# Kernel optimization log

Hardware: AMD Instinct MI355X
Metric: run time of the kernel (lower is better)

The kernel has to match this reference:

```python
import jax, jax.numpy as jnp
import numpy as np

N = 100000
E = 1600000
F_IN = 128
HID = 64
HID2 = 32
NCLS = 2
EPS = 1e-5  # BatchNorm eps


def setup_inputs() -> dict:
    key = jax.random.key(0)
    ks = jax.random.split(key, 12)
    inp = {
        'x': jax.random.normal(ks[0], (N, F_IN), dtype=jnp.float32),
        'edge_index': jax.random.randint(ks[1], (2, E), 0, N, dtype=jnp.int64),
        # GCNConv layer 1: weight [F_IN, HID], bias [HID]
        'W1': jax.random.normal(ks[2], (F_IN, HID), dtype=jnp.float32) / np.sqrt(F_IN),
        'b1': jnp.zeros((HID,), dtype=jnp.float32),
        # GCNConv layer 2
        'W2': jax.random.normal(ks[3], (HID, HID2), dtype=jnp.float32) / np.sqrt(HID),
        'b2': jnp.zeros((HID2,), dtype=jnp.float32),
        # BatchNorm1d params (eval mode: running stats)
        'g1': jax.random.uniform(ks[4], (HID,), dtype=jnp.float32, minval=0.5, maxval=1.5),
        'be1': jax.random.normal(ks[5], (HID,), dtype=jnp.float32) * 0.1,
        'rm1': jax.random.normal(ks[6], (HID,), dtype=jnp.float32) * 0.1,
        'rv1': jax.random.uniform(ks[7], (HID,), dtype=jnp.float32, minval=0.5, maxval=1.5),
        'g2': jax.random.uniform(ks[8], (HID2,), dtype=jnp.float32, minval=0.5, maxval=1.5),
        'be2': jax.random.normal(ks[9], (HID2,), dtype=jnp.float32) * 0.1,
        'rm2': jax.random.normal(ks[10], (HID2,), dtype=jnp.float32) * 0.1,
        'rv2': jax.random.uniform(ks[11], (HID2,), dtype=jnp.float32, minval=0.5, maxval=1.5),
        # classifier
        'Wc': jax.random.normal(jax.random.fold_in(key, 99), (HID2, NCLS), dtype=jnp.float32) / np.sqrt(HID2),
        'bc': jnp.zeros((NCLS,), dtype=jnp.float32),
    }
    return inp


def _gcn_conv(x, src, dst, norm, W, b, n_nodes):
    # PyG GCNConv: transform -> gather source -> norm-weight -> scatter-add -> +bias
    h = x @ W                                  # [N, out]
    msg = h[src] * norm[:, None]               # [E+N, out] gathered messages
    out = jax.ops.segment_sum(msg, dst, num_segments=n_nodes)
    return out + b


def _bn_eval(x, gamma, beta, rmean, rvar):
    return (x - rmean) * (gamma * jax.lax.rsqrt(rvar + EPS)) + beta


def reference(x, edge_index, W1, b1, W2, b2, g1, be1, rm1, rv1, g2, be2, rm2, rv2, Wc, bc):
    n = x.shape[0]
    loop = jnp.arange(n, dtype=edge_index.dtype)
    src = jnp.concatenate([edge_index[0], loop])   # add self-loops
    dst = jnp.concatenate([edge_index[1], loop])
    # symmetric degree normalization on A + I (degree counted at target)
    deg = jax.ops.segment_sum(jnp.ones_like(dst, dtype=x.dtype), dst, num_segments=n)
    dinv = jnp.where(deg > 0, jax.lax.rsqrt(deg), 0.0)
    norm = dinv[src] * dinv[dst]                   # [E+N]

    h = _gcn_conv(x, src, dst, norm, W1, b1, n)
    h = jax.nn.relu(_bn_eval(h, g1, be1, rm1, rv1))
    # dropout: identity in eval mode
    h = _gcn_conv(h, src, dst, norm, W2, b2, n)
    h = jax.nn.relu(_bn_eval(h, g2, be2, rm2, rv2))
    logits = h @ Wc + bc
    return jax.nn.log_softmax(logits, axis=1)
```

## Files before the change

kernel.cpp:

```cpp
#include <hip/hip_runtime.h>
#include <hip/hip_fp16.h>
#include <math.h>

#define F_IN 128
#define HID 64
#define HID2 32
#define EPS_BN 1e-5f
#define BW 128
#define NBMAX 1024
#define CAP 2560
#define CH 8192

__global__ __launch_bounds__(1024) void partition_kernel(const int* __restrict__ src, const int* __restrict__ dst,
                                                         int E, int* __restrict__ gcursor,
                                                         unsigned* __restrict__ ebuf) {
    __shared__ int hist[NBMAX];
    __shared__ int start[NBMAX];
    __shared__ int cur[NBMAX];
    __shared__ int gb[NBMAX];
    __shared__ int sc[1024];
    __shared__ unsigned buf[CH];
    int tid = threadIdx.x;
    int e0 = blockIdx.x * CH;
    hist[tid] = 0;
    __syncthreads();
#pragma unroll
    for (int it = 0; it < CH / 1024; it++) {
        int e = e0 + tid + it * 1024;
        if (e < E) atomicAdd(&hist[dst[e] >> 7], 1);
    }
    __syncthreads();
    int v = hist[tid];
    sc[tid] = v;
    __syncthreads();
    for (int off = 1; off < 1024; off <<= 1) {
        int t = (tid >= off) ? sc[tid - off] : 0;
        __syncthreads();
        sc[tid] += t;
        __syncthreads();
    }
    int ex = sc[tid] - v;
    start[tid] = ex;
    cur[tid] = ex;
    gb[tid] = v ? atomicAdd(&gcursor[tid], v) : 0;
    __syncthreads();
#pragma unroll
    for (int it = 0; it < CH / 1024; it++) {
        int e = e0 + tid + it * 1024;
        if (e < E) {
            int d = dst[e], s = src[e];
            int p = atomicAdd(&cur[d >> 7], 1);
            buf[p] = ((unsigned)(d & (BW - 1)) << 17) | (unsigned)s;
        }
    }
    __syncthreads();
    int grp = tid >> 2, sub = tid & 3;
    for (int b = grp; b < NBMAX; b += 256) {
        int len = hist[b];
        if (!len) continue;
        int st = start[b];
        unsigned* dp = ebuf + (size_t)b * CAP + gb[b];
        for (int i = sub; i < len; i += 4) dp[i] = buf[st + i];
    }
}

__global__ __launch_bounds__(256) void localsort_kernel(unsigned* __restrict__ ebuf, const int* __restrict__ gcursor,
                                                        int* __restrict__ ns, int* __restrict__ ne,
                                                        float* __restrict__ dinv, int n) {
    __shared__ unsigned lbuf[CAP];
    __shared__ int lhist[BW];
    __shared__ int lcur[BW];
    __shared__ int stmp[256];
    int b = blockIdx.x;
    int tid = threadIdx.x;
    int base = b * CAP;
    int len = gcursor[b];
    int node0 = b * BW;
    int nn = min(BW, n - node0);
    if (tid < BW) lhist[tid] = 0;
    __syncthreads();
    for (int k = tid; k < len; k += 256) {
        unsigned u = ebuf[base + k];
        lbuf[k] = u;
        atomicAdd(&lhist[u >> 17], 1);
    }
    __syncthreads();
    int v = (tid < BW) ? lhist[tid] : 0;
    stmp[tid] = v;
    __syncthreads();
    for (int off = 1; off < 256; off <<= 1) {
        int t = (tid >= off) ? stmp[tid - off] : 0;
        __syncthreads();
        stmp[tid] += t;
        __syncthreads();
    }
    int ex = stmp[tid] - v;
    if (tid < BW) lcur[tid] = ex;
    if (tid < nn) {
        ns[node0 + tid] = base + ex;
        ne[node0 + tid] = base + ex + v;
        dinv[node0 + tid] = rsqrtf((float)(v + 1));
    }
    __syncthreads();
    for (int k = tid; k < len; k += 256) {
        unsigned u = lbuf[k];
        int p = atomicAdd(&lcur[u >> 17], 1);
        ebuf[base + p] = u & 0x1FFFFu;
    }
}

__global__ void constprep_kernel(const float* g1, const float* be1, const float* rm1, const float* rv1, const float* b1,
                                 const float* g2, const float* be2, const float* rm2, const float* rv2, const float* b2,
                                 float* A1, float* B1, float* A2, float* B2) {
    int t = threadIdx.x;
    if (t < HID)  { float s = g1[t] * rsqrtf(rv1[t] + EPS_BN); A1[t] = s; B1[t] = (b1[t] - rm1[t]) * s + be1[t]; }
    if (t < HID2) { float s = g2[t] * rsqrtf(rv2[t] + EPS_BN); A2[t] = s; B2[t] = (b2[t] - rm2[t]) * s + be2[t]; }
}

__global__ __launch_bounds__(256, 5) void gemm1_kernel(const float* __restrict__ x, const float* __restrict__ W1,
                                                       const float* __restrict__ dinv, __half* __restrict__ ht1,
                                                       int n) {
    __shared__ float wlds[F_IN * HID];
    int tid = threadIdx.x;
    {
        const float4* wv = (const float4*)W1;
        float4* wl = (float4*)wlds;
#pragma unroll
        for (int i = 0; i < F_IN * HID / 4 / 256; i++) wl[tid + 256 * i] = wv[tid + 256 * i];
    }
    __syncthreads();
    int row0 = blockIdx.x * 64;
    int col4 = (tid & 15) * 4;
    int rowg = tid >> 4;
    const float* xr[4];
#pragma unroll
    for (int r = 0; r < 4; r++) {
        int rr = row0 + rowg * 4 + r;
        xr[r] = x + (size_t)min(rr, n - 1) * F_IN;
    }
    float acc[4][4];
#pragma unroll
    for (int r = 0; r < 4; r++)
#pragma unroll
        for (int c = 0; c < 4; c++) acc[r][c] = 0.f;
#pragma unroll 4
    for (int k = 0; k < F_IN; k += 4) {
        float4 xa[4];
#pragma unroll
        for (int r = 0; r < 4; r++) xa[r] = *(const float4*)(xr[r] + k);
        float4 wb[4];
#pragma unroll
        for (int j = 0; j < 4; j++) wb[j] = *(const float4*)&wlds[(k + j) * HID + col4];
#pragma unroll
        for (int r = 0; r < 4; r++) {
            acc[r][0] = fmaf(xa[r].x, wb[0].x, acc[r][0]); acc[r][1] = fmaf(xa[r].x, wb[0].y, acc[r][1]);
            acc[r][2] = fmaf(xa[r].x, wb[0].z, acc[r][2]); acc[r][3] = fmaf(xa[r].x, wb[0].w, acc[r][3]);
            acc[r][0] = fmaf(xa[r].y, wb[1].x, acc[r][0]); acc[r][1] = fmaf(xa[r].y, wb[1].y, acc[r][1]);
            acc[r][2] = fmaf(xa[r].y, wb[1].z, acc[r][2]); acc[r][3] = fmaf(xa[r].y, wb[1].w, acc[r][3]);
            acc[r][0] = fmaf(xa[r].z, wb[2].x, acc[r][0]); acc[r][1] = fmaf(xa[r].z, wb[2].y, acc[r][1]);
            acc[r][2] = fmaf(xa[r].z, wb[2].z, acc[r][2]); acc[r][3] = fmaf(xa[r].z, wb[2].w, acc[r][3]);
            acc[r][0] = fmaf(xa[r].w, wb[3].x, acc[r][0]); acc[r][1] = fmaf(xa[r].w, wb[3].y, acc[r][1]);
            acc[r][2] = fmaf(xa[r].w, wb[3].z, acc[r][2]); acc[r][3] = fmaf(xa[r].w, wb[3].w, acc[r][3]);
        }
    }
    int rbase = row0 + rowg * 4;
#pragma unroll
    for (int r = 0; r < 4; r++) {
        int row = rbase + r;
        if (row < n) {
            float d = dinv[row];
            __half2 h0, h1;
            h0.x = __float2half(acc[r][0] * d); h0.y = __float2half(acc[r][1] * d);
            h1.x = __float2half(acc[r][2] * d); h1.y = __float2half(acc[r][3] * d);
            __half2* dp = (__half2*)(ht1 + (size_t)row * HID + col4);
            dp[0] = h0; dp[1] = h1;
        }
    }
}

#define XP2 68
__global__ __launch_bounds__(256) void gemm2_kernel(const float* __restrict__ h1p, const float* __restrict__ W2,
                                                    const float* __restrict__ dinv, __half* __restrict__ ht2,
                                                    int n) {
    __shared__ float wlds[HID * HID2];
    __shared__ float xlds[64 * XP2];
    int tid = threadIdx.x;
    {
        const float4* wv = (const float4*)W2;
        float4* wl = (float4*)wlds;
#pragma unroll
        for (int i = 0; i < HID * HID2 / 4 / 256; i++) wl[tid + 256 * i] = wv[tid + 256 * i];
    }
    int row0 = blockIdx.x * 64;
    {
        const float4* xv = (const float4*)(h1p + (size_t)row0 * HID);
        int lim = (n - row0) * (HID / 4);
#pragma unroll
        for (int i = 0; i < 4; i++) {
            int f = tid + 256 * i;
            float4 v = make_float4(0.f, 0.f, 0.f, 0.f);
            if (f < lim) v = xv[f];
            int r = f >> 4, kp = (f & 15) * 4;
            *(float4*)&xlds[r * XP2 + kp] = v;
        }
    }
    __syncthreads();
    int col4 = (tid & 7) * 4;
    int rowg = tid >> 3;
    float acc[2][4];
#pragma unroll
    for (int r = 0; r < 2; r++)
#pragma unroll
        for (int c = 0; c < 4; c++) acc[r][c] = 0.f;
#pragma unroll 4
    for (int k = 0; k < HID; k += 4) {
        float4 wb[4];
#pragma unroll
        for (int j = 0; j < 4; j++) wb[j] = *(const float4*)&wlds[(k + j) * HID2 + col4];
#pragma unroll
        for (int r = 0; r < 2; r++) {
            float4 xa = *(const float4*)&xlds[(rowg * 2 + r) * XP2 + k];
            acc[r][0] = fmaf(xa.x, wb[0].x, acc[r][0]); acc[r][1] = fmaf(xa.x, wb[0].y, acc[r][1]);
            acc[r][2] = fmaf(xa.x, wb[0].z, acc[r][2]); acc[r][3] = fmaf(xa.x, wb[0].w, acc[r][3]);
            acc[r][0] = fmaf(xa.y, wb[1].x, acc[r][0]); acc[r][1] = fmaf(xa.y, wb[1].y, acc[r][1]);
            acc[r][2] = fmaf(xa.y, wb[1].z, acc[r][2]); acc[r][3] = fmaf(xa.y, wb[1].w, acc[r][3]);
            acc[r][0] = fmaf(xa.z, wb[2].x, acc[r][0]); acc[r][1] = fmaf(xa.z, wb[2].y, acc[r][1]);
            acc[r][2] = fmaf(xa.z, wb[2].z, acc[r][2]); acc[r][3] = fmaf(xa.z, wb[2].w, acc[r][3]);
            acc[r][0] = fmaf(xa.w, wb[3].x, acc[r][0]); acc[r][1] = fmaf(xa.w, wb[3].y, acc[r][1]);
            acc[r][2] = fmaf(xa.w, wb[3].z, acc[r][2]); acc[r][3] = fmaf(xa.w, wb[3].w, acc[r][3]);
        }
    }
    int rbase = row0 + rowg * 2;
#pragma unroll
    for (int r = 0; r < 2; r++) {
        int row = rbase + r;
        if (row < n) {
            float d = dinv[row];
            __half2 h0, h1;
            h0.x = __float2half(acc[r][0] * d); h0.y = __float2half(acc[r][1] * d);
            h1.x = __float2half(acc[r][2] * d); h1.y = __float2half(acc[r][3] * d);
            __half2* dp = (__half2*)(ht2 + (size_t)row * HID2 + col4);
            dp[0] = h0; dp[1] = h1;
        }
    }
}

__global__ __launch_bounds__(256) void agg1_kernel(const __half* __restrict__ ht1, const int* __restrict__ ns,
                                                   const int* __restrict__ ne, const int* __restrict__ csr,
                                                   const float* __restrict__ dinv,
                                                   const float* __restrict__ A1, const float* __restrict__ B1,
                                                   float* __restrict__ h1p, int n) {
    int node = (blockIdx.x * blockDim.x + threadIdx.x) >> 6;
    if (node >= n) return;
    int lane = threadIdx.x & 63;
    int eh = lane >> 5, cp = lane & 31;
    const __half2* htp = (const __half2*)ht1;
    int s = ns[node], e_end = ne[node];
    float ax = 0.f, ay = 0.f;
    if (eh == 0) {
        float2 f = __half22float2(htp[(size_t)node * 32 + cp]);
        ax = f.x; ay = f.y;
    }
    for (int i = s + eh; i < e_end; i += 16) {
        int idx[8];
        bool val[8];
#pragma unroll
        for (int j = 0; j < 8; j++) {
            int e = i + 2 * j;
            val[j] = e < e_end;
            idx[j] = csr[val[j] ? e : s];
        }
#pragma unroll
        for (int j = 0; j < 8; j++) {
            float2 f = __half22float2(htp[(size_t)idx[j] * 32 + cp]);
            ax += val[j] ? f.x : 0.f;
            ay += val[j] ? f.y : 0.f;
        }
    }
    ax += __shfl_xor(ax, 32);
    ay += __shfl_xor(ay, 32);
    if (eh == 0) {
        float d = dinv[node];
        int c0 = cp * 2;
        float2 o;
        o.x = fmaxf(fmaf(ax * d, A1[c0], B1[c0]), 0.f);
        o.y = fmaxf(fmaf(ay * d, A1[c0 + 1], B1[c0 + 1]), 0.f);
        *(float2*)&h1p[(size_t)node * HID + c0] = o;
    }
}

__global__ __launch_bounds__(256) void agg2_kernel(const __half* __restrict__ ht2, const int* __restrict__ ns,
                                                   const int* __restrict__ ne, const int* __restrict__ csr,
                                                   const float* __restrict__ dinv,
                                                   const float* __restrict__ A2, const float* __restrict__ B2,
                                                   const float* __restrict__ Wc, const float* __restrict__ bc,
                                                   float* __restrict__ out, int n) {
    int node = (blockIdx.x * blockDim.x + threadIdx.x) >> 6;
    if (node >= n) return;
    int lane = threadIdx.x & 63;
    int eq = lane >> 4, cp = lane & 15;
    const __half2* htp = (const __half2*)ht2;
    int s = ns[node], e_end = ne[node];
    float ax = 0.f, ay = 0.f;
    if (eq == 0) {
        float2 f = __half22float2(htp[(size_t)node * 16 + cp]);
        ax = f.x; ay = f.y;
    }
    for (int i = s + eq; i < e_end; i += 16) {
        int idx[4];
        bool val[4];
#pragma unroll
        for (int j = 0; j < 4; j++) {
            int e = i + 4 * j;
            val[j] = e < e_end;
            idx[j] = csr[val[j] ? e : s];
        }
#pragma unroll
        for (int j = 0; j < 4; j++) {
            float2 f = __half22float2(htp[(size_t)idx[j] * 16 + cp]);
            ax += val[j] ? f.x : 0.f;
            ay += val[j] ? f.y : 0.f;
        }
    }
    ax += __shfl_xor(ax, 32); ay += __shfl_xor(ay, 32);
    ax += __shfl_xor(ax, 16); ay += __shfl_xor(ay, 16);
    float d = dinv[node];
    int c0 = cp * 2;
    float v0 = fmaxf(fmaf(ax * d, A2[c0], B2[c0]), 0.f);
    float v1 = fmaxf(fmaf(ay * d, A2[c0 + 1], B2[c0 + 1]), 0.f);
    float p0 = v0 * Wc[c0 * 2 + 0] + v1 * Wc[c0 * 2 + 2];
    float p1 = v0 * Wc[c0 * 2 + 1] + v1 * Wc[c0 * 2 + 3];
#pragma unroll
    for (int off = 8; off >= 1; off >>= 1) { p0 += __shfl_xor(p0, off); p1 += __shfl_xor(p1, off); }
    if (lane == 0) {
        float l0 = p0 + bc[0], l1 = p1 + bc[1];
        float m = fmaxf(l0, l1);
        float lse = m + logf(expf(l0 - m) + expf(l1 - m));
        float2 o; o.x = l0 - lse; o.y = l1 - lse;
        *(float2*)&out[(size_t)node * 2] = o;
    }
}

extern "C" void kernel_launch(void* const* d_in, const int* in_sizes, int n_in,
                              void* d_out, int out_size, void* d_ws, size_t ws_size,
                              hipStream_t stream) {
    const float* x   = (const float*)d_in[0];
    const int*   ei  = (const int*)d_in[1];
    const float* W1  = (const float*)d_in[2];
    const float* b1  = (const float*)d_in[3];
    const float* W2  = (const float*)d_in[4];
    const float* b2  = (const float*)d_in[5];
    const float* g1  = (const float*)d_in[6];
    const float* be1 = (const float*)d_in[7];
    const float* rm1 = (const float*)d_in[8];
    const float* rv1 = (const float*)d_in[9];
    const float* g2  = (const float*)d_in[10];
    const float* be2 = (const float*)d_in[11];
    const float* rm2 = (const float*)d_in[12];
    const float* rv2 = (const float*)d_in[13];
    const float* Wc  = (const float*)d_in[14];
    const float* bc  = (const float*)d_in[15];
    float* out = (float*)d_out;

    int n = in_sizes[0] / F_IN;
    int E = in_sizes[1] / 2;
    const int* srcv = ei;
    const int* dstv = ei + E;
    int NB = (n + BW - 1) / BW;

    char* ws = (char*)d_ws;
    size_t off = 0;
    auto alloc = [&](size_t bytes) -> char* {
        char* r = ws + off;
        off = (off + bytes + 511) & ~(size_t)511;
        return r;
    };
    int*      gcursor = (int*)alloc((size_t)NB * 4);
    int*      ns      = (int*)alloc((size_t)n * 4);
    int*      ne      = (int*)alloc((size_t)n * 4);
    float*    dinv    = (float*)alloc((size_t)n * 4);
    float*    A1 = (float*)alloc(HID * 4);
    float*    B1 = (float*)alloc(HID * 4);
    float*    A2 = (float*)alloc(HID2 * 4);
    float*    B2 = (float*)alloc(HID2 * 4);
    unsigned* ebuf = (unsigned*)alloc((size_t)NB * CAP * 4);
    __half*   ht1  = (__half*)alloc((size_t)n * HID * 2);
    float*    h1p  = (float*)alloc((size_t)n * HID * 4);
    __half*   ht2  = ht1;

    hipMemsetAsync(gcursor, 0, (size_t)NB * 4, stream);

    int nch = (E + CH - 1) / CH;
    partition_kernel<<<nch, 1024, 0, stream>>>(srcv, dstv, E, gcursor, ebuf);
    localsort_kernel<<<NB, 256, 0, stream>>>(ebuf, gcursor, ns, ne, dinv, n);
    constprep_kernel<<<1, 64, 0, stream>>>(g1, be1, rm1, rv1, b1, g2, be2, rm2, rv2, b2, A1, B1, A2, B2);

    int ngb = (n + 63) / 64;
    gemm1_kernel<<<ngb, 256, 0, stream>>>(x, W1, dinv, ht1, n);
    agg1_kernel<<<(n + 3) / 4, 256, 0, stream>>>(ht1, ns, ne, (const int*)ebuf, dinv, A1, B1, h1p, n);
    gemm2_kernel<<<ngb, 256, 0, stream>>>(h1p, W2, dinv, ht2, n);
    agg2_kernel<<<(n + 3) / 4, 256, 0, stream>>>(ht2, ns, ne, (const int*)ebuf, dinv, A2, B2, Wc, bc, out, n);
}
```

Measured before the change: 272.1 us.

## Compute first GCN linear transform with fp16 MFMA in a persistent grid

Replaces the scalar FMA register-tiled GEMM for x@W1 with MFMA 16x16x32 fp16 instructions. W1 fragments are converted to half and held in registers, and each wave loops over 16-row tiles in a fixed 512-block persistent grid. This aims to cut ALU time in the first transform, at the cost of rounding x and W1 to fp16 before accumulation and of using narrower 2-byte scattered output stores.

```diff
diff --git a/kernel.cpp b/kernel.cpp
--- a/kernel.cpp
+++ b/kernel.cpp
@@ -10,6 +10,9 @@
 #define NBMAX 1024
 #define CAP 2560
 #define CH 8192
+
+typedef _Float16 f16x8 __attribute__((ext_vector_type(8)));
+typedef float f32x4 __attribute__((ext_vector_type(4)));
 
 __global__ __launch_bounds__(1024) void partition_kernel(const int* __restrict__ src, const int* __restrict__ dst,
                                                          int E, int* __restrict__ gcursor,
@@ -117,9 +120,9 @@
     if (t < HID2) { float s = g2[t] * rsqrtf(rv2[t] + EPS_BN); A2[t] = s; B2[t] = (b2[t] - rm2[t]) * s + be2[t]; }
 }
 
-__global__ __launch_bounds__(256, 5) void gemm1_kernel(const float* __restrict__ x, const float* __restrict__ W1,
-                                                       const float* __restrict__ dinv, __half* __restrict__ ht1,
-                                                       int n) {
+__global__ __launch_bounds__(256) void gemm1_kernel(const float* __restrict__ x, const float* __restrict__ W1,
+                                                    const float* __restrict__ dinv, __half* __restrict__ ht1,
+                                                    int n, int nwaves_tot) {
     __shared__ float wlds[F_IN * HID];
     int tid = threadIdx.x;
     {
@@ -129,51 +132,51 @@
         for (int i = 0; i < F_IN * HID / 4 / 256; i++) wl[tid + 256 * i] = wv[tid + 256 * i];
     }
     __syncthreads();
-    int row0 = blockIdx.x * 64;
-    int col4 = (tid & 15) * 4;
-    int rowg = tid >> 4;
-    const float* xr[4];
-#pragma unroll
-    for (int r = 0; r < 4; r++) {
-        int rr = row0 + rowg * 4 + r;
-        xr[r] = x + (size_t)min(rr, n - 1) * F_IN;
-    }
-    float acc[4][4];
-#pragma unroll
-    for (int r = 0; r < 4; r++)
-#pragma unroll
-        for (int c = 0; c < 4; c++) acc[r][c] = 0.f;
-#pragma unroll 4
-    for (int k = 0; k < F_IN; k += 4) {
-        float4 xa[4];
-#pragma unroll
-        for (int r = 0; r < 4; r++) xa[r] = *(const float4*)(xr[r] + k);
-        float4 wb[4];
-#pragma unroll
-        for (int j = 0; j < 4; j++) wb[j] = *(const float4*)&wlds[(k + j) * HID + col4];
-#pragma unroll
-        for (int r = 0; r < 4; r++) {
-            acc[r][0] = fmaf(xa[r].x, wb[0].x, acc[r][0]); acc[r][1] = fmaf(xa[r].x, wb[0].y, acc[r][1]);
-            acc[r][2] = fmaf(xa[r].x, wb[0].z, acc[r][2]); acc[r][3] = fmaf(xa[r].x, wb[0].w, acc[r][3]);
-            acc[r][0] = fmaf(xa[r].y, wb[1].x, acc[r][0]); acc[r][1] = fmaf(xa[r].y, wb[1].y, acc[r][1]);
-            acc[r][2] = fmaf(xa[r].y, wb[1].z, acc[r][2]); acc[r][3] = fmaf(xa[r].y, wb[1].w, acc[r][3]);
-            acc[r][0] = fmaf(xa[r].z, wb[2].x, acc[r][0]); acc[r][1] = fmaf(xa[r].z, wb[2].y, acc[r][1]);
-            acc[r][2] = fmaf(xa[r].z, wb[2].z, acc[r][2]); acc[r][3] = fmaf(xa[r].z, wb[2].w, acc[r][3]);
-            acc[r][0] = fmaf(xa[r].w, wb[3].x, acc[r][0]); acc[r][1] = fmaf(xa[r].w, wb[3].y, acc[r][1]);
-            acc[r][2] = fmaf(xa[r].w, wb[3].z, acc[r][2]); acc[r][3] = fmaf(xa[r].w, wb[3].w, acc[r][3]);
-        }
-    }
-    int rbase = row0 + rowg * 4;
-#pragma unroll
-    for (int r = 0; r < 4; r++) {
-        int row = rbase + r;
-        if (row < n) {
-            float d = dinv[row];
-            __half2 h0, h1;
-            h0.x = __float2half(acc[r][0] * d); h0.y = __float2half(acc[r][1] * d);
-            h1.x = __float2half(acc[r][2] * d); h1.y = __float2half(acc[r][3] * d);
-            __half2* dp = (__half2*)(ht1 + (size_t)row * HID + col4);
-            dp[0] = h0; dp[1] = h1;
+    int lane = tid & 63;
+    int l15 = lane & 15, lg = lane >> 4;
+    f16x8 bf[4][4];
+#pragma unroll
+    for (int ks = 0; ks < 4; ks++) {
+#pragma unroll
+        for (int ct = 0; ct < 4; ct++) {
+            int kb = ks * 32 + lg * 8;
+            int col = ct * 16 + l15;
+            f16x8 b;
+#pragma unroll
+            for (int e = 0; e < 8; e++) b[e] = (_Float16)wlds[(kb + e) * HID + col];
+            bf[ks][ct] = b;
+        }
+    }
+    int gw = blockIdx.x * 4 + (tid >> 6);
+    int nrt = (n + 15) >> 4;
+    for (int rt = gw; rt < nrt; rt += nwaves_tot) {
+        int arow = rt * 16 + l15;
+        const float* xr = x + (size_t)min(arow, n - 1) * F_IN;
+        f32x4 acc[4];
+#pragma unroll
+        for (int ct = 0; ct < 4; ct++) acc[ct] = (f32x4){0.f, 0.f, 0.f, 0.f};
+#pragma unroll
+        for (int ks = 0; ks < 4; ks++) {
+            float4 xa = *(const float4*)(xr + ks * 32 + lg * 8);
+            float4 xb = *(const float4*)(xr + ks * 32 + lg * 8 + 4);
+            f16x8 a;
+            a[0] = (_Float16)xa.x; a[1] = (_Float16)xa.y; a[2] = (_Float16)xa.z; a[3] = (_Float16)xa.w;
+            a[4] = (_Float16)xb.x; a[5] = (_Float16)xb.y; a[6] = (_Float16)xb.z; a[7] = (_Float16)xb.w;
+#pragma unroll
+            for (int ct = 0; ct < 4; ct++)
+                acc[ct] = __builtin_amdgcn_mfma_f32_16x16x32_f16(a, bf[ks][ct], acc[ct], 0, 0, 0);
+        }
+        int rbase = rt * 16 + lg * 4;
+#pragma unroll
+        for (int reg = 0; reg < 4; reg++) {
+            int row = rbase + reg;
+            if (row < n) {
+                float d = dinv[row];
+                _Float16* dp = (_Float16*)ht1 + (size_t)row * HID + l15;
+#pragma unroll
+                for (int ct = 0; ct < 4; ct++)
+                    dp[ct * 16] = (_Float16)(acc[ct][reg] * d);
+            }
         }
     }
 }
@@ -395,9 +398,10 @@
     localsort_kernel<<<NB, 256, 0, stream>>>(ebuf, gcursor, ns, ne, dinv, n);
     constprep_kernel<<<1, 64, 0, stream>>>(g1, be1, rm1, rv1, b1, g2, be2, rm2, rv2, b2, A1, B1, A2, B2);
 
+    int g1blocks = 512;
+    gemm1_kernel<<<g1blocks, 256, 0, stream>>>(x, W1, dinv, ht1, n, g1blocks * 4);
+    agg1_kernel<<<(n + 3) / 4, 256, 0, stream>>>(ht1, ns, ne, (const int*)ebuf, dinv, A1, B1, h1p, n);
     int ngb = (n + 63) / 64;
-    gemm1_kernel<<<ngb, 256, 0, stream>>>(x, W1, dinv, ht1, n);
-    agg1_kernel<<<(n + 3) / 4, 256, 0, stream>>>(ht1, ns, ne, (const int*)ebuf, dinv, A1, B1, h1p, n);
     gemm2_kernel<<<ngb, 256, 0, stream>>>(h1p, W2, dinv, ht2, n);
     agg2_kernel<<<(n + 3) / 4, 256, 0, stream>>>(ht2, ns, ne, (const int*)ebuf, dinv, A2, B2, Wc, bc, out, n);
 }
```

After: 253.8 us. 6.7% less time.
